# Performance work log

Hardware: AMD Instinct MI355X
Metric: run time of the kernel (lower is better)

## Reference

```python
import jax, jax.numpy as jnp
import numpy as np

NUM_HEADS = 12

def setup_inputs() -> dict:
    key = jax.random.key(0)
    k1, k2, k3 = jax.random.split(key, 3)
    dim = 768
    x = jax.random.normal(k1, (1, 64, 64, dim), dtype=jnp.float32)
    qkv_w = jax.random.normal(k2, (3 * dim, dim), dtype=jnp.float32) * (dim ** -0.5)
    qkv_b = jnp.zeros((3 * dim,), dtype=jnp.float32)
    proj_w = jax.random.normal(k3, (dim, dim), dtype=jnp.float32) * (dim ** -0.5)
    proj_b = jnp.zeros((dim,), dtype=jnp.float32)
    return {"x": x, "qkv_w": qkv_w, "qkv_b": qkv_b, "proj_w": proj_w, "proj_b": proj_b}

def reference(x, qkv_w, qkv_b, proj_w, proj_b):
    B, H, W, C = x.shape
    N = H * W
    nh = NUM_HEADS
    # qkv projection: [B,H,W,3C] -> [B,N,3,nh,hd]
    qkv = jnp.einsum('bhwc,dc->bhwd', x, qkv_w) + qkv_b
    qkv = qkv.reshape(B, N, 3, nh, -1)
    q, k, v = qkv[:, :, 0], qkv[:, :, 1], qkv[:, :, 2]  # [B,N,nh,hd]
    q = q.transpose(0, 2, 1, 3)  # [B,nh,N,hd]
    k = k.transpose(0, 2, 1, 3)
    v = v.transpose(0, 2, 1, 3)
    hd = q.shape[-1]
    scale = hd ** -0.5
    scores = jnp.einsum('bhnd,bhmd->bhnm', q, k) * scale  # [B,nh,N,N]
    attn = jax.nn.softmax(scores.astype(jnp.float32), axis=-1).astype(q.dtype)
    attn = jax.lax.stop_gradient(attn)
    out = jnp.einsum('bhnm,bhmd->bhnd', attn, v)  # [B,nh,N,hd]
    out = out.transpose(0, 2, 1, 3).reshape(B, H, W, -1)
    out = jnp.einsum('bhwc,dc->bhwd', out, proj_w) + proj_b
    return out
```

## Files before the change

### kernel.cpp

```cpp
#include <hip/hip_runtime.h>

typedef short short8 __attribute__((ext_vector_type(8)));
typedef short short2v __attribute__((ext_vector_type(2)));
typedef float f32x4 __attribute__((ext_vector_type(4)));
typedef float f32x16 __attribute__((ext_vector_type(16)));
typedef unsigned short ushort4v __attribute__((ext_vector_type(4)));
typedef unsigned int u32;
typedef unsigned int u32x4 __attribute__((ext_vector_type(4)));

__device__ __forceinline__ unsigned short f2b(float f) {
  unsigned u = __builtin_bit_cast(unsigned, f);
  u = u + 0x7FFFu + ((u >> 16) & 1u);
  return (unsigned short)(u >> 16);
}

__global__ void f2bf3_kernel(const float* __restrict__ a, unsigned short* __restrict__ oa, int na,
                             const float* __restrict__ b, unsigned short* __restrict__ ob, int nb,
                             const float* __restrict__ c, unsigned short* __restrict__ oc, int nc) {
  int i = blockIdx.x * blockDim.x + threadIdx.x;
  const float* in; unsigned short* out;
  if (i < na)           { in = a; out = oa; }
  else if (i < na + nb) { i -= na; in = b; out = ob; }
  else if (i < na + nb + nc) { i -= na + nb; in = c; out = oc; }
  else return;
  float4 v = reinterpret_cast<const float4*>(in)[i];
  ushort4v o;
  o.x = f2b(v.x); o.y = f2b(v.y); o.z = f2b(v.z); o.w = f2b(v.w);
  reinterpret_cast<ushort4v*>(out)[i] = o;
}

__device__ __forceinline__ void store_out(float* C, int idx, float v) { C[idx] = v; }
__device__ __forceinline__ void store_out(short* C, int idx, float v) { C[idx] = (short)f2b(v); }

template <typename OutT>
__global__ __launch_bounds__(256, 2)
void gemm_bt_kernel(const short* __restrict__ A, const short* __restrict__ B,
                    const float* __restrict__ bias, OutT* __restrict__ C,
                    int M, int N, int K, int qcols, float qscale)
{
  __shared__ __align__(16) short lds_a[128][72];
  __shared__ __align__(16) short lds_b[128][72];

  const int tid  = threadIdx.x;
  const int lane = tid & 63;
  const int wave = tid >> 6;
  const int wm   = wave >> 1;
  const int wn   = wave & 1;
  const int r16  = lane & 15;
  const int q4   = lane >> 4;
  const int bm   = blockIdx.x;
  const int bn   = blockIdx.y;

  f32x4 zero = {0.f, 0.f, 0.f, 0.f};
  f32x4 acc[4][4];
#pragma unroll
  for (int i = 0; i < 4; ++i)
#pragma unroll
    for (int j = 0; j < 4; ++j) acc[i][j] = zero;

  const int srow = tid >> 3;
  const int scol = (tid & 7) * 8;
  const short* Ab = A + (bm * 128 + srow) * K + scol;
  const short* Bb = B + (bn * 128 + srow) * K + scol;

  short8 ar[4], br[4];
#pragma unroll
  for (int i = 0; i < 4; ++i) {
    ar[i] = *reinterpret_cast<const short8*>(Ab + i * 32 * K);
    br[i] = *reinterpret_cast<const short8*>(Bb + i * 32 * K);
  }

  const int nk = K >> 6;
  for (int kt = 0; kt < nk; ++kt) {
#pragma unroll
    for (int i = 0; i < 4; ++i) {
      *reinterpret_cast<short8*>(&lds_a[srow + i * 32][scol]) = ar[i];
      *reinterpret_cast<short8*>(&lds_b[srow + i * 32][scol]) = br[i];
    }
    __syncthreads();
    if (kt + 1 < nk) {
      const short* An = Ab + (kt + 1) * 64;
      const short* Bn = Bb + (kt + 1) * 64;
#pragma unroll
      for (int i = 0; i < 4; ++i) {
        ar[i] = *reinterpret_cast<const short8*>(An + i * 32 * K);
        br[i] = *reinterpret_cast<const short8*>(Bn + i * 32 * K);
      }
    }
#pragma unroll
    for (int kk = 0; kk < 2; ++kk) {
      short8 af[4], bf[4];
#pragma unroll
      for (int mi = 0; mi < 4; ++mi)
        af[mi] = *reinterpret_cast<const short8*>(&lds_a[wm * 64 + mi * 16 + r16][kk * 32 + q4 * 8]);
#pragma unroll
      for (int ni = 0; ni < 4; ++ni)
        bf[ni] = *reinterpret_cast<const short8*>(&lds_b[wn * 64 + ni * 16 + r16][kk * 32 + q4 * 8]);
#pragma unroll
      for (int mi = 0; mi < 4; ++mi)
#pragma unroll
        for (int ni = 0; ni < 4; ++ni)
          acc[mi][ni] = __builtin_amdgcn_mfma_f32_16x16x32_bf16(af[mi], bf[ni], acc[mi][ni], 0, 0, 0);
    }
    __syncthreads();
  }

#pragma unroll
  for (int mi = 0; mi < 4; ++mi) {
    const int row0 = bm * 128 + wm * 64 + mi * 16 + q4 * 4;
#pragma unroll
    for (int ni = 0; ni < 4; ++ni) {
      const int col = bn * 128 + wn * 64 + ni * 16 + r16;
      const float bz = bias[col];
      const float sc = (col < qcols) ? qscale : 1.f;
#pragma unroll
      for (int j = 0; j < 4; ++j)
        store_out(C, (row0 + j) * N + col, (acc[mi][ni][j] + bz) * sc);
    }
  }
}

__global__ __launch_bounds__(256, 3)
void attn_kernel(const short* __restrict__ QKV, short* __restrict__ Ao)
{
  constexpr int C3 = 2304;
  __shared__ __align__(16) short k_lds[2][64][64];
  __shared__ __align__(16) short v_lds[2][2][64][64];

  const int tid  = threadIdx.x;
  const int lane = tid & 63;
  const int wave = tid >> 6;
  const int sp   = wave >> 1;
  const int qh   = wave & 1;
  const int l31  = lane & 31;
  const int hi   = lane >> 5;
  const int swz  = l31 & 7;
  const int h    = blockIdx.y;
  const int qt   = blockIdx.x;

  const short* Qp = QKV + h * 64;

  const int qrow = qt * 64 + qh * 32 + l31;
  short8 qf[4];
#pragma unroll
  for (int ks = 0; ks < 4; ++ks)
    qf[ks] = *reinterpret_cast<const short8*>(Qp + qrow * C3 + ks * 16 + hi * 8);

  const int t2 = tid & 127;
  const int kr = t2 >> 3;
  const int kc = t2 & 7;
  const int kswz = 8 * (kc ^ (kr & 7));

  const short* Kt = QKV + 768  + h * 64 + (size_t)(sp * 2048 + kr)     * C3 + kc * 8;
  const short* Vt = QKV + 1536 + h * 64 + (size_t)(sp * 2048 + 2 * kr) * C3 + kc * 8;

  short8 ka[4], va[4];
  auto LOADT = [&]() {
#pragma unroll
    for (int j = 0; j < 4; ++j)
      ka[j] = *reinterpret_cast<const short8*>(Kt + j * 16 * C3);
    va[0] = *reinterpret_cast<const short8*>(Vt);
    va[1] = *reinterpret_cast<const short8*>(Vt + C3);
    va[2] = *reinterpret_cast<const short8*>(Vt + 32 * C3);
    va[3] = *reinterpret_cast<const short8*>(Vt + 33 * C3);
    Kt += 64 * C3; Vt += 64 * C3;
  };

  const int vb3_0 = (2 * kr) >> 3, vko = (2 * kr) & 7;

  short* const vw0 = &v_lds[sp][0][0][0];
  short* const vw1 = &v_lds[sp][1][0][0];
  short* vwr = vw0;
  short* vww = vw1;

  auto WRITET = [&](short* vb) {
#pragma unroll
    for (int j = 0; j < 4; ++j)
      *reinterpret_cast<short8*>(&k_lds[sp][kr + 16 * j][kswz]) = ka[j];
#pragma unroll
    for (int p = 0; p < 2; ++p) {
      const int b3 = vb3_0 + 4 * p;
#pragma unroll
      for (int i = 0; i < 8; ++i) {
        short2v pr; pr.x = va[2 * p][i]; pr.y = va[2 * p + 1][i];
        *reinterpret_cast<short2v*>(vb + (kc * 8 + i) * 64 + 8 * (b3 ^ kc ^ i) + vko) = pr;
      }
    }
  };

  const f32x16 ZEROv = {};
  const short ONE_BF = (short)0x3F80;
  const short8 ONESv = {ONE_BF, ONE_BF, ONE_BF, ONE_BF, ONE_BF, ONE_BF, ONE_BF, ONE_BF};

  f32x16 o0 = {}, o1 = {}, acc_l = {};

  LOADT();
  WRITET(vw0);
  LOADT();
  __syncthreads();

  for (int kt = 0; kt < 32; ++kt) {
    f32x16 s0, s1;
    {
      const short* kb0 = &k_lds[sp][l31][0];
      const short* kb1 = &k_lds[sp][l31 + 32][0];
      __builtin_amdgcn_s_setprio(1);
#pragma unroll
      for (int ks = 0; ks < 4; ++ks) {
        const int off = 8 * (((ks << 1) | hi) ^ swz);
        short8 kf0 = *reinterpret_cast<const short8*>(kb0 + off);
        short8 kf1 = *reinterpret_cast<const short8*>(kb1 + off);
        s0 = __builtin_amdgcn_mfma_f32_32x32x16_bf16(kf0, qf[ks], ks ? s0 : ZEROv, 0, 0, 0);
        s1 = __builtin_amdgcn_mfma_f32_32x32x16_bf16(kf1, qf[ks], ks ? s1 : ZEROv, 0, 0, 0);
      }
      __builtin_amdgcn_s_setprio(0);
    }
    __syncthreads();

    if (kt != 31) {
      WRITET(vww);
      if (kt != 30) LOADT();
    }

#pragma unroll
    for (int i = 0; i < 16; ++i) { s0[i] = exp2f(s0[i]); s1[i] = exp2f(s1[i]); }

    u32 pkv[4][4];
#pragma unroll
    for (int t = 0; t < 4; ++t) {
      asm("v_cvt_pk_bf16_f32 %0, %1, %2" : "=v"(pkv[0][t]) : "v"(s0[2 * t]),     "v"(s0[2 * t + 1]));
      asm("v_cvt_pk_bf16_f32 %0, %1, %2" : "=v"(pkv[1][t]) : "v"(s0[8 + 2 * t]), "v"(s0[8 + 2 * t + 1]));
      asm("v_cvt_pk_bf16_f32 %0, %1, %2" : "=v"(pkv[2][t]) : "v"(s1[2 * t]),     "v"(s1[2 * t + 1]));
      asm("v_cvt_pk_bf16_f32 %0, %1, %2" : "=v"(pkv[3][t]) : "v"(s1[8 + 2 * t]), "v"(s1[8 + 2 * t + 1]));
    }
#pragma unroll
    for (int ks = 0; ks < 4; ++ks) {
      asm("v_permlane32_swap_b32 %0, %1" : "+v"(pkv[ks][0]), "+v"(pkv[ks][2]));
      asm("v_permlane32_swap_b32 %0, %1" : "+v"(pkv[ks][1]), "+v"(pkv[ks][3]));
    }
    short8 pa[4];
#pragma unroll
    for (int ks = 0; ks < 4; ++ks) {
      u32x4 tmp = {pkv[ks][0], pkv[ks][1], pkv[ks][2], pkv[ks][3]};
      pa[ks] = __builtin_bit_cast(short8, tmp);
    }

#pragma unroll
    for (int ks = 0; ks < 4; ++ks)
      acc_l = __builtin_amdgcn_mfma_f32_32x32x16_bf16(pa[ks], ONESv, acc_l, 0, 0, 0);

    {
      const short* vb0 = vwr + l31 * 64;
      const short* vb1 = vwr + (l31 + 32) * 64;
      const int rsw = (l31 >> 3) ^ (l31 & 7);
      __builtin_amdgcn_s_setprio(1);
#pragma unroll
      for (int ks = 0; ks < 4; ++ks) {
        const int c = ((ks << 1) | hi) ^ rsw;
        short8 vf0 = *reinterpret_cast<const short8*>(vb0 + 8 * c);
        short8 vf1 = *reinterpret_cast<const short8*>(vb1 + 8 * (c ^ 4));
        o0 = __builtin_amdgcn_mfma_f32_32x32x16_bf16(pa[ks], vf0, o0, 0, 0, 0);
        o1 = __builtin_amdgcn_mfma_f32_32x32x16_bf16(pa[ks], vf1, o1, 0, 0, 0);
      }
      __builtin_amdgcn_s_setprio(0);
    }

    { short* t = vwr; vwr = vww; vww = t; }
    __syncthreads();
  }

  float* o_sh = (float*)&k_lds[0][0][0];
  float* l_sh = (float*)&v_lds[0][0][0][0];

  if (sp == 1) {
#pragma unroll
    for (int r = 0; r < 16; ++r) {
      const int q = (r & 3) + 8 * (r >> 2) + 4 * hi;
      const int row = qh * 32 + q;
      o_sh[row * 64 + l31]      = o0[r];
      o_sh[row * 64 + 32 + l31] = o1[r];
    }
    if (l31 == 0) {
#pragma unroll
      for (int r = 0; r < 16; ++r) {
        const int q = (r & 3) + 8 * (r >> 2) + 4 * hi;
        l_sh[qh * 32 + q] = acc_l[r];
      }
    }
  }
  __syncthreads();
  if (sp == 0) {
#pragma unroll
    for (int r = 0; r < 16; ++r) {
      const int q = (r & 3) + 8 * (r >> 2) + 4 * hi;
      const int row = qh * 32 + q;
      const float lt = 1.f / (acc_l[r] + l_sh[row]);
      const int grow = qt * 64 + row;
      float a0 = (o0[r] + o_sh[row * 64 + l31]) * lt;
      float a1 = (o1[r] + o_sh[row * 64 + 32 + l31]) * lt;
      Ao[grow * 768 + h * 64 + l31]      = (short)f2b(a0);
      Ao[grow * 768 + h * 64 + 32 + l31] = (short)f2b(a1);
    }
  }
}

extern "C" void kernel_launch(void* const* d_in, const int* in_sizes, int n_in,
                              void* d_out, int out_size, void* d_ws, size_t ws_size,
                              hipStream_t stream)
{
  const float* x      = (const float*)d_in[0];
  const float* qkv_w  = (const float*)d_in[1];
  const float* qkv_b  = (const float*)d_in[2];
  const float* proj_w = (const float*)d_in[3];
  const float* proj_b = (const float*)d_in[4];
  float* out = (float*)d_out;

  char* ws = (char*)d_ws;
  short* xb  = (short*)(ws + 0);
  short* wq  = (short*)(ws + 6291456);
  short* wp  = (short*)(ws + 9830400);
  short* qkv = (short*)(ws + 11010048);
  short* ao  = (short*)(ws + 29884416);

  const float sscale = 0.125f * 1.44269504088896340736f;

  f2bf3_kernel<<<5376, 256, 0, stream>>>(x, (unsigned short*)xb, 786432,
                                         qkv_w, (unsigned short*)wq, 442368,
                                         proj_w, (unsigned short*)wp, 147456);

  gemm_bt_kernel<short><<<dim3(32, 18), 256, 0, stream>>>(xb, wq, qkv_b, qkv, 4096, 2304, 768, 768, sscale);
  attn_kernel<<<dim3(64, 12), 256, 0, stream>>>(qkv, ao);
  gemm_bt_kernel<float><<<dim3(32, 6), 256, 0, stream>>>(ao, wp, proj_b, out, 4096, 768, 768, 0, 1.f);
}
```

Before: 147.1 us.

## Load K directly from global and give each wave a private V transpose buffer

The attention loop no longer stages K in shared LDS: each wave reads its K fragments straight from global memory into registers. V is transposed into a per-wave private LDS region instead of a double-buffered buffer shared by the block, which removes the two block-wide barriers per iteration. In exchange, waves with the same key split now each fetch the same K and V tiles redundantly from global/L2, V loads are exposed with less prefetch distance, and register pressure rises.

```diff
diff --git a/kernel.cpp b/kernel.cpp
--- a/kernel.cpp
+++ b/kernel.cpp
@@ -124,8 +124,7 @@
 void attn_kernel(const short* __restrict__ QKV, short* __restrict__ Ao)
 {
   constexpr int C3 = 2304;
-  __shared__ __align__(16) short k_lds[2][64][64];
-  __shared__ __align__(16) short v_lds[2][2][64][64];
+  __shared__ __align__(16) short v_priv[4][64][64];
 
   const int tid  = threadIdx.x;
   const int lane = tid & 63;
@@ -134,97 +133,75 @@
   const int qh   = wave & 1;
   const int l31  = lane & 31;
   const int hi   = lane >> 5;
-  const int swz  = l31 & 7;
   const int h    = blockIdx.y;
   const int qt   = blockIdx.x;
 
-  const short* Qp = QKV + h * 64;
-
   const int qrow = qt * 64 + qh * 32 + l31;
   short8 qf[4];
 #pragma unroll
   for (int ks = 0; ks < 4; ++ks)
-    qf[ks] = *reinterpret_cast<const short8*>(Qp + qrow * C3 + ks * 16 + hi * 8);
-
-  const int t2 = tid & 127;
-  const int kr = t2 >> 3;
-  const int kc = t2 & 7;
-  const int kswz = 8 * (kc ^ (kr & 7));
-
-  const short* Kt = QKV + 768  + h * 64 + (size_t)(sp * 2048 + kr)     * C3 + kc * 8;
-  const short* Vt = QKV + 1536 + h * 64 + (size_t)(sp * 2048 + 2 * kr) * C3 + kc * 8;
-
-  short8 ka[4], va[4];
-  auto LOADT = [&]() {
-#pragma unroll
-    for (int j = 0; j < 4; ++j)
-      ka[j] = *reinterpret_cast<const short8*>(Kt + j * 16 * C3);
-    va[0] = *reinterpret_cast<const short8*>(Vt);
-    va[1] = *reinterpret_cast<const short8*>(Vt + C3);
-    va[2] = *reinterpret_cast<const short8*>(Vt + 32 * C3);
-    va[3] = *reinterpret_cast<const short8*>(Vt + 33 * C3);
-    Kt += 64 * C3; Vt += 64 * C3;
-  };
-
-  const int vb3_0 = (2 * kr) >> 3, vko = (2 * kr) & 7;
-
-  short* const vw0 = &v_lds[sp][0][0][0];
-  short* const vw1 = &v_lds[sp][1][0][0];
-  short* vwr = vw0;
-  short* vww = vw1;
-
-  auto WRITET = [&](short* vb) {
-#pragma unroll
-    for (int j = 0; j < 4; ++j)
-      *reinterpret_cast<short8*>(&k_lds[sp][kr + 16 * j][kswz]) = ka[j];
-#pragma unroll
-    for (int p = 0; p < 2; ++p) {
-      const int b3 = vb3_0 + 4 * p;
-#pragma unroll
-      for (int i = 0; i < 8; ++i) {
-        short2v pr; pr.x = va[2 * p][i]; pr.y = va[2 * p + 1][i];
-        *reinterpret_cast<short2v*>(vb + (kc * 8 + i) * 64 + 8 * (b3 ^ kc ^ i) + vko) = pr;
-      }
-    }
-  };
+    qf[ks] = *reinterpret_cast<const short8*>(QKV + h * 64 + qrow * C3 + ks * 16 + hi * 8);
+
+  const short* Kt  = QKV + 768 + h * 64 + (size_t)(sp * 2048 + l31) * C3 + hi * 8;
+  const short* Kt2 = Kt + 32 * C3;
+
+  const int kr3 = (lane >> 3) & 7;
+  const int kc3 = lane & 7;
+  const short* Vt = QKV + 1536 + h * 64 + (size_t)(sp * 2048 + 2 * kr3) * C3 + kc3 * 8;
+
+  short* const vp = &v_priv[wave][0][0];
+  const int vko = 2 * (kr3 & 3);
+  const int vb3 = kr3 >> 2;
+
+  short8 va[8];
+
+#pragma unroll
+  for (int j = 0; j < 4; ++j) {
+    va[2 * j]     = *reinterpret_cast<const short8*>(Vt + (16 * j) * C3);
+    va[2 * j + 1] = *reinterpret_cast<const short8*>(Vt + (16 * j + 1) * C3);
+  }
+  Vt += 64 * C3;
 
   const f32x16 ZEROv = {};
   const short ONE_BF = (short)0x3F80;
   const short8 ONESv = {ONE_BF, ONE_BF, ONE_BF, ONE_BF, ONE_BF, ONE_BF, ONE_BF, ONE_BF};
+  const int rsw = (l31 >> 3) ^ (l31 & 7);
 
   f32x16 o0 = {}, o1 = {}, acc_l = {};
 
-  LOADT();
-  WRITET(vw0);
-  LOADT();
-  __syncthreads();
-
   for (int kt = 0; kt < 32; ++kt) {
+    short8 kf0[4], kf1[4];
+#pragma unroll
+    for (int ks = 0; ks < 4; ++ks) {
+      kf0[ks] = *reinterpret_cast<const short8*>(Kt  + ks * 16);
+      kf1[ks] = *reinterpret_cast<const short8*>(Kt2 + ks * 16);
+    }
+    Kt += 64 * C3; Kt2 += 64 * C3;
+
+    asm volatile("s_waitcnt lgkmcnt(0)" ::: "memory");
+    __builtin_amdgcn_sched_barrier(0);
+
+#pragma unroll
+    for (int j = 0; j < 4; ++j) {
+      const int b3 = vb3 + 2 * j;
+#pragma unroll
+      for (int i = 0; i < 8; ++i) {
+        short2v pr; pr.x = va[2 * j][i]; pr.y = va[2 * j + 1][i];
+        *reinterpret_cast<short2v*>(vp + (kc3 * 8 + i) * 64 + 8 * (b3 ^ kc3 ^ i) + vko) = pr;
+      }
+    }
+
     f32x16 s0, s1;
-    {
-      const short* kb0 = &k_lds[sp][l31][0];
-      const short* kb1 = &k_lds[sp][l31 + 32][0];
-      __builtin_amdgcn_s_setprio(1);
-#pragma unroll
-      for (int ks = 0; ks < 4; ++ks) {
-        const int off = 8 * (((ks << 1) | hi) ^ swz);
-        short8 kf0 = *reinterpret_cast<const short8*>(kb0 + off);
-        short8 kf1 = *reinterpret_cast<const short8*>(kb1 + off);
-        s0 = __builtin_amdgcn_mfma_f32_32x32x16_bf16(kf0, qf[ks], ks ? s0 : ZEROv, 0, 0, 0);
-        s1 = __builtin_amdgcn_mfma_f32_32x32x16_bf16(kf1, qf[ks], ks ? s1 : ZEROv, 0, 0, 0);
-      }
-      __builtin_amdgcn_s_setprio(0);
-    }
-    __syncthreads();
-
-    if (kt != 31) {
-      WRITET(vww);
-      if (kt != 30) LOADT();
-    }
+    __builtin_amdgcn_s_setprio(1);
+#pragma unroll
+    for (int ks = 0; ks < 4; ++ks) {
+      s0 = __builtin_amdgcn_mfma_f32_32x32x16_bf16(kf0[ks], qf[ks], ks ? s0 : ZEROv, 0, 0, 0);
+      s1 = __builtin_amdgcn_mfma_f32_32x32x16_bf16(kf1[ks], qf[ks], ks ? s1 : ZEROv, 0, 0, 0);
+    }
+    __builtin_amdgcn_s_setprio(0);
 
 #pragma unroll
     for (int i = 0; i < 16; ++i) { s0[i] = exp2f(s0[i]); s1[i] = exp2f(s1[i]); }
-
     u32 pkv[4][4];
 #pragma unroll
     for (int t = 0; t < 4; ++t) {
@@ -245,32 +222,46 @@
       pa[ks] = __builtin_bit_cast(short8, tmp);
     }
 
+    if (kt != 31) {
+#pragma unroll
+      for (int j = 0; j < 4; ++j) {
+        va[2 * j]     = *reinterpret_cast<const short8*>(Vt + (16 * j) * C3);
+        va[2 * j + 1] = *reinterpret_cast<const short8*>(Vt + (16 * j + 1) * C3);
+      }
+      Vt += 64 * C3;
+    }
+
+    asm volatile("s_waitcnt lgkmcnt(0)" ::: "memory");
+    __builtin_amdgcn_sched_barrier(0);
+
+    short8 vf0[4], vf1[4];
+    {
+      const short* vb0 = vp + l31 * 64;
+      const short* vb1 = vp + (l31 + 32) * 64;
+#pragma unroll
+      for (int ks = 0; ks < 4; ++ks) {
+        const int c = ((ks << 1) | hi) ^ rsw;
+        vf0[ks] = *reinterpret_cast<const short8*>(vb0 + 8 * c);
+        vf1[ks] = *reinterpret_cast<const short8*>(vb1 + 8 * (c ^ 4));
+      }
+    }
+
 #pragma unroll
     for (int ks = 0; ks < 4; ++ks)
       acc_l = __builtin_amdgcn_mfma_f32_32x32x16_bf16(pa[ks], ONESv, acc_l, 0, 0, 0);
-
-    {
-      const short* vb0 = vwr + l31 * 64;
-      const short* vb1 = vwr + (l31 + 32) * 64;
-      const int rsw = (l31 >> 3) ^ (l31 & 7);
-      __builtin_amdgcn_s_setprio(1);
-#pragma unroll
-      for (int ks = 0; ks < 4; ++ks) {
-        const int c = ((ks << 1) | hi) ^ rsw;
-        short8 vf0 = *reinterpret_cast<const short8*>(vb0 + 8 * c);
-        short8 vf1 = *reinterpret_cast<const short8*>(vb1 + 8 * (c ^ 4));
-        o0 = __builtin_amdgcn_mfma_f32_32x32x16_bf16(pa[ks], vf0, o0, 0, 0, 0);
-        o1 = __builtin_amdgcn_mfma_f32_32x32x16_bf16(pa[ks], vf1, o1, 0, 0, 0);
-      }
-      __builtin_amdgcn_s_setprio(0);
-    }
-
-    { short* t = vwr; vwr = vww; vww = t; }
-    __syncthreads();
-  }
-
-  float* o_sh = (float*)&k_lds[0][0][0];
-  float* l_sh = (float*)&v_lds[0][0][0][0];
+    __builtin_amdgcn_s_setprio(1);
+#pragma unroll
+    for (int ks = 0; ks < 4; ++ks) {
+      o0 = __builtin_amdgcn_mfma_f32_32x32x16_bf16(pa[ks], vf0[ks], o0, 0, 0, 0);
+      o1 = __builtin_amdgcn_mfma_f32_32x32x16_bf16(pa[ks], vf1[ks], o1, 0, 0, 0);
+    }
+    __builtin_amdgcn_s_setprio(0);
+  }
+
+  __syncthreads();
+
+  float* o_sh = (float*)&v_priv[0][0][0];
+  float* l_sh = (float*)&v_priv[2][0][0];
 
   if (sp == 1) {
 #pragma unroll
```

Measured after the change: 324.7 us. 2.21x slower.
